# Kernel tuning notes

Measured on AMD Instinct MI355X. Metric: run time of the kernel, lower is better.

## Reference

```python
import math
import jax, jax.numpy as jnp
import numpy as np

N_HEAD = 16
ROPE_BASE = 10000.0


def _rope_tables(T, half, dtype):
    # build_sin_cos(seq_len, dim=head_dim//2): inv freq of length `half`
    pos = jnp.arange(T, dtype=jnp.float32)[:, None]                      # [T,1]
    inv = jnp.exp(jnp.arange(0, half * 2, 2, dtype=jnp.float32) * (-math.log(ROPE_BASE) / (half * 2)))  # [half]
    ang = pos * inv                                                       # [T,half]
    return jnp.sin(ang).astype(dtype), jnp.cos(ang).astype(dtype)


def setup_inputs() -> dict:
    key = jax.random.key(0)
    k1, k2, k3 = jax.random.split(key, 3)
    B, T, C = 2, 2048, 2048
    x = jax.random.normal(k1, (B, T, C), dtype=jnp.float32)
    w_qkv = jax.random.normal(k2, (3 * C, C), dtype=jnp.float32) * (1.0 / math.sqrt(C))
    w_proj = jax.random.normal(k3, (C, C), dtype=jnp.float32) * (1.0 / math.sqrt(C))
    return {"x": x, "w_qkv": w_qkv, "w_proj": w_proj}


def reference(x, w_qkv, w_proj):
    B, T, C = x.shape
    H = N_HEAD
    D = C // H
    half = D // 2

    qkv = jnp.einsum('btc,fc->btf', x, w_qkv).reshape(B, T, 3, H, D)
    q, k, v = qkv[:, :, 0], qkv[:, :, 1], qkv[:, :, 2]   # [B,T,H,D]

    sin, cos = _rope_tables(T, half, x.dtype)            # [T,half]
    sin = sin[None, :, None, :]                          # [1,T,1,half]
    cos = cos[None, :, None, :]

    def rot(t):
        t1, t2 = t[..., :half], t[..., half:]
        return jnp.concatenate([t1 * cos - t2 * sin, t2 * cos + t1 * sin], axis=-1)

    q, k = rot(q), rot(k)

    scale = 1.0 / math.sqrt(D)
    scores = jnp.einsum('bthd,bshd->bhts', q, k) * scale  # [B,H,T,T]
    causal = jnp.tril(jnp.ones((T, T), dtype=bool))
    scores = jnp.where(causal[None, None], scores, jnp.finfo(scores.dtype).min)
    probs = jax.nn.softmax(scores, axis=-1)
    out = jnp.einsum('bhts,bshd->bhtd', probs, v)         # [B,H,T,D]

    # Faithful to torch: view(B,T,H,D).permute(0,2,1,3).reshape_as(x)
    # flash output is token-major (B,T,H,D); permute gives (B,H,T,D), then flat reshape to (B,T,C).
    out = out.reshape(B, T, C)
    return jnp.einsum('btc,oc->bto', out, w_proj)
```

## Files before the change

kernel.cpp:

```cpp
#include <hip/hip_runtime.h>
#include <math.h>

typedef __attribute__((ext_vector_type(8))) short short8;
typedef __attribute__((ext_vector_type(4))) float f32x4;
typedef __attribute__((ext_vector_type(16))) float f32x16;
typedef __attribute__((ext_vector_type(4))) unsigned short ushort4v;
typedef __attribute__((ext_vector_type(2))) int int2v;

#define AS1 __attribute__((address_space(1)))
#define AS3 __attribute__((address_space(3)))
#define GLOAD16(src, dst) __builtin_amdgcn_global_load_lds((const AS1 void*)(src), (AS3 void*)(dst), 16, 0, 0)
#define VMWAIT(N) asm volatile("s_waitcnt vmcnt(" #N ")" ::: "memory")
#define LGKM0()   asm volatile("s_waitcnt lgkmcnt(0)" ::: "memory")

__device__ __forceinline__ unsigned short f2b(float f) {
    union { float f; unsigned int u; } c; c.f = f;
    return (unsigned short)((c.u + 0x7FFFu + ((c.u >> 16) & 1u)) >> 16);
}
__device__ __forceinline__ float b2f(unsigned short u) {
    union { unsigned int u; float f; } c; c.u = ((unsigned int)u) << 16;
    return c.f;
}
__device__ __forceinline__ int cvt_pk_bf16(float a, float b) {
    int r;
    asm("v_cvt_pk_bf16_f32 %0, %1, %2" : "=v"(r) : "v"(a), "v"(b));
    return r;
}
__device__ __forceinline__ int xcd_swz(int id, int nwg) {
    int q = nwg >> 3, r = nwg & 7, x = id & 7, rest = id >> 3;
    return (x < r ? x * (q + 1) : r * (q + 1) + (x - r) * q) + rest;
}

__global__ void cvt2(const float* __restrict__ a, const float* __restrict__ bsrc,
                     unsigned short* __restrict__ dst, int n4a) {
    int f = blockIdx.x * 256 + threadIdx.x;
    float4 v = (f < n4a) ? ((const float4*)a)[f] : ((const float4*)bsrc)[f - n4a];
    ushort4v o;
    o.x = f2b(v.x); o.y = f2b(v.y); o.z = f2b(v.z); o.w = f2b(v.w);
    ((ushort4v*)dst)[f] = o;
}

__global__ __launch_bounds__(256) void mid_fused(unsigned short* __restrict__ qkv,
                                                 unsigned short* __restrict__ vtg,
                                                 const float* __restrict__ wproj,
                                                 unsigned short* __restrict__ wpb) {
    int bid = blockIdx.x;
    if (bid < 16384) {
        int tid = bid * 256 + threadIdx.x;
        int i = tid & 63;
        int h = (tid >> 6) & 15;
        int t = (tid >> 10) & 2047;
        int b = tid >> 21;
        float inv = __expf((float)i * -0.14391156608f);
        float ang = (float)t * inv;
        float sn = sinf(ang), cs = cosf(ang);
        size_t base0 = ((size_t)(((b << 11) + t) * 3)) << 11;
#pragma unroll
        for (int s = 0; s < 2; ++s) {
            size_t base = base0 + (size_t)s * 2048 + (h << 7);
            float v1 = b2f(qkv[base + i]);
            float v2 = b2f(qkv[base + 64 + i]);
            qkv[base + i]      = f2b(v1 * cs - v2 * sn);
            qkv[base + 64 + i] = f2b(v2 * cs + v1 * sn);
        }
    } else if (bid < 16384 + 4096) {
        int flat = (bid - 16384) * 256 + threadIdx.x;
        int t = flat & 2047;
        int dc = (flat >> 11) & 15;
        int h = (flat >> 15) & 15;
        int b = flat >> 19;
        short8 v = *(const short8*)(qkv + ((size_t)(b * 2048 + t) * 3 + 2) * 2048 + h * 128 + dc * 8);
        size_t base = ((size_t)(b * 16 + h) * 128 + dc * 8) * 2048 + t;
#pragma unroll
        for (int j = 0; j < 8; j++) vtg[base + (size_t)j * 2048] = (unsigned short)v[j];
    } else {
        int f = (bid - 20480) * 256 + threadIdx.x;
#pragma unroll
        for (int r = 0; r < 4; ++r, f += 1024 * 256) {
            float4 v = ((const float4*)wproj)[f];
            ushort4v o;
            o.x = f2b(v.x); o.y = f2b(v.y); o.z = f2b(v.z); o.w = f2b(v.w);
            ((ushort4v*)wpb)[f] = o;
        }
    }
}

template<int OUT_BF16>
__global__ __launch_bounds__(512, 2) void gemm_nt(const unsigned short* __restrict__ A,
                                                  const unsigned short* __restrict__ B,
                                                  void* __restrict__ Cout,
                                                  int N, int K) {
    __shared__ __attribute__((aligned(16))) char lds[73728];
    int tid = threadIdx.x, lane = tid & 63, w = tid >> 6;
    int col = lane & 15, lg = lane >> 4;
    int wr = w >> 2, wc = w & 3;
    int gx = gridDim.x;
    int nwg = gx * gridDim.y;
    int id = xcd_swz(blockIdx.y * gx + blockIdx.x, nwg);
    int rowBase = (id / gx) * 128;
    int colBase = (id % gx) * 256;
    int nkt = K >> 5;

    f32x4 acc[4][4];
#pragma unroll
    for (int m = 0; m < 4; m++)
#pragma unroll
        for (int n = 0; n < 4; n++) acc[m][n] = (f32x4){0.f, 0.f, 0.f, 0.f};

    auto slotOf = [&](int t) { return t - (t / 3) * 3; };

    auto stageA = [&](int t) {
        char* dst = lds + slotOf(t) * 8192 + w * 1024;
        int u = w * 64 + lane;
        int row = u >> 2, ch = u & 3;
        const char* src = (const char*)A + ((size_t)(rowBase + row) * K + t * 32) * 2
                          + (((ch ^ (row >> 1)) & 3) << 4);
        GLOAD16(src, dst);
    };
    auto stageB = [&](int t) {
        char* base = lds + 24576 + slotOf(t) * 16384;
#pragma unroll
        for (int j = 0; j < 2; ++j) {
            int u = j * 512 + w * 64 + lane;
            int row = u >> 2, ch = u & 3;
            const char* src = (const char*)B + ((size_t)(colBase + row) * K + t * 32) * 2
                              + (((ch ^ (row >> 1)) & 3) << 4);
            GLOAD16(src, base + j * 8192 + w * 1024);
        }
    };

    stageA(0); stageB(0); stageA(1); stageB(1);

    for (int t = 0; t < nkt; ++t) {
        if (t + 1 < nkt) VMWAIT(3);
        else             VMWAIT(0);
        __builtin_amdgcn_s_barrier();
        if (t + 2 < nkt) { stageA(t + 2); stageB(t + 2); }
        const char* Ab = lds + slotOf(t) * 8192;
        const char* Bb = lds + 24576 + slotOf(t) * 16384;
        short8 af[4], bf[4];
#pragma unroll
        for (int m = 0; m < 4; ++m) {
            int row = wr * 64 + m * 16 + col;
            af[m] = *(const short8*)(Ab + row * 64 + (((lg ^ (row >> 1)) & 3) << 4));
        }
#pragma unroll
        for (int n = 0; n < 4; ++n) {
            int row = wc * 64 + n * 16 + col;
            bf[n] = *(const short8*)(Bb + row * 64 + (((lg ^ (row >> 1)) & 3) << 4));
        }
        __builtin_amdgcn_s_setprio(1);
#pragma unroll
        for (int m = 0; m < 4; ++m)
#pragma unroll
            for (int n = 0; n < 4; ++n)
                acc[m][n] = __builtin_amdgcn_mfma_f32_16x16x32_bf16(af[m], bf[n], acc[m][n], 0, 0, 0);
        __builtin_amdgcn_s_setprio(0);
        LGKM0();
    }

    int rbase = 4 * lg;
#pragma unroll
    for (int m = 0; m < 4; m++)
#pragma unroll
        for (int reg = 0; reg < 4; ++reg) {
            int r = rowBase + wr * 64 + m * 16 + rbase + reg;
#pragma unroll
            for (int n = 0; n < 4; n++) {
                int c = colBase + wc * 64 + n * 16 + col;
                float v = acc[m][n][reg];
                if (OUT_BF16) ((unsigned short*)Cout)[(size_t)r * N + c] = f2b(v);
                else          ((float*)Cout)[(size_t)r * N + c] = v;
            }
        }
}

__global__ __launch_bounds__(256, 2) void attn_fused(const unsigned short* __restrict__ qkv,
                                                     const unsigned short* __restrict__ vtg,
                                                     unsigned short* __restrict__ out) {
    constexpr int T = 2048;
    __shared__ unsigned short Kl[2][64 * 128];
    __shared__ unsigned short Vl[2][128 * 64];
    int tid = threadIdx.x, lane = tid & 63, w = tid >> 6;
    int q = lane & 31, hi = lane >> 5;
    int id = blockIdx.x;
    int bh = id & 31;
    int u = (id >> 5) & 7;
    int qt = (id >> 8) ? (15 - u) : u;
    int b = bh >> 4, h = bh & 15;
    const float sc2 = 0.08838834764831845f * 1.44269504088896340f;

    int qbase = qt * 128;
    int nkv = 2 * qt + 2;
    int tq = qbase + w * 32 + q;

    short8 qf[8];
    {
        const unsigned short* qp = qkv + ((size_t)(b * T + tq) * 3) * 2048 + h * 128;
#pragma unroll
        for (int s = 0; s < 8; s++) qf[s] = *(const short8*)(qp + s * 16 + hi * 8);
    }
    f32x16 O[4];
#pragma unroll
    for (int dt = 0; dt < 4; dt++)
#pragma unroll
        for (int r = 0; r < 16; r++) O[dt][r] = 0.f;
    float m = -1e30f, l = 0.f;

    auto stageK = [&](int t) {
        int kvb = t * 64;
        char* Kb = (char*)&Kl[t & 1][0];
#pragma unroll
        for (int it = 0; it < 4; ++it) {
            int dby = it * 4096 + tid * 16;
            int row = dby >> 8, cb = dby & 255;
            int scb = cb ^ ((row & 7) << 4);
            const char* src = (const char*)qkv + (((size_t)(b * T + kvb + row) * 3 + 1) * 2048 + h * 128) * 2 + scb;
            GLOAD16(src, Kb + it * 4096 + w * 1024);
        }
    };
    auto stageV = [&](int t) {
        int kvb = t * 64;
        char* Vb = (char*)&Vl[t & 1][0];
#pragma unroll
        for (int it = 0; it < 4; ++it) {
            int dby = it * 4096 + tid * 16;
            int d = dby >> 7, cb = dby & 127;
            int scb = cb ^ ((d & 7) << 4);
            const char* src = (const char*)vtg + (((size_t)bh * 128 + d) * 2048 + kvb) * 2 + scb;
            GLOAD16(src, Vb + it * 4096 + w * 1024);
        }
    };

    stageK(0); stageV(0);

    for (int kv = 0; kv < nkv; ++kv) {
        if (kv + 1 < nkv) {
            stageK(kv + 1);
            stageV(kv + 1);
            VMWAIT(8);
        } else {
            VMWAIT(0);
        }
        __builtin_amdgcn_s_barrier();
        int kvbase = kv * 64;
        bool act = kvbase < qbase + (w + 1) * 32;
        const char* Kb = (const char*)&Kl[kv & 1][0];
        const char* Vb = (const char*)&Vl[kv & 1][0];
        if (act) {
            f32x16 p0, p1;
#pragma unroll
            for (int r = 0; r < 16; r++) { p0[r] = 0.f; p1[r] = 0.f; }
            __builtin_amdgcn_s_setprio(1);
#pragma unroll
            for (int s = 0; s < 8; s++) {
                int cb = s * 32 + hi * 16;
                short8 k0 = *(const short8*)(Kb + q * 256 + (cb ^ ((q & 7) << 4)));
                p0 = __builtin_amdgcn_mfma_f32_32x32x16_bf16(k0, qf[s], p0, 0, 0, 0);
                short8 k1 = *(const short8*)(Kb + (32 + q) * 256 + (cb ^ ((q & 7) << 4)));
                p1 = __builtin_amdgcn_mfma_f32_32x32x16_bf16(k1, qf[s], p1, 0, 0, 0);
            }
            __builtin_amdgcn_s_setprio(0);
#pragma unroll
            for (int r = 0; r < 16; r++) { p0[r] *= sc2; p1[r] *= sc2; }
            bool diag = (kvbase + 63 > qbase + w * 32);
            if (diag) {
#pragma unroll
                for (int r = 0; r < 16; r++) {
                    int kg = kvbase + (r & 3) + 8 * (r >> 2) + 4 * hi;
                    if (kg > tq) p0[r] = -3e38f;
                    if (kg + 32 > tq) p1[r] = -3e38f;
                }
            }
            float mx = -3e38f;
#pragma unroll
            for (int r = 0; r < 16; r++) mx = fmaxf(mx, fmaxf(p0[r], p1[r]));
            mx = fmaxf(mx, __shfl_xor(mx, 32));
            if (!__all(mx - m <= 8.0f)) {
                float mn = fmaxf(m, mx);
                float esc = exp2f(m - mn);
                m = mn;
                l *= esc;
#pragma unroll
                for (int dt = 0; dt < 4; dt++)
#pragma unroll
                    for (int r = 0; r < 16; r++) O[dt][r] *= esc;
            }
            float rs = 0.f;
#pragma unroll
            for (int r = 0; r < 16; r++) {
                p0[r] = exp2f(p0[r] - m); rs += p0[r];
                p1[r] = exp2f(p1[r] - m); rs += p1[r];
            }
            rs += __shfl_xor(rs, 32);
            l += rs;
            union Frag { int i[4]; short8 s; } pa[4];
#pragma unroll
            for (int g = 0; g < 4; g++) {
                float e[8];
#pragma unroll
                for (int j = 0; j < 8; j++) e[j] = (g < 2) ? p0[(g & 1) * 8 + j] : p1[(g & 1) * 8 + j];
                int a0 = cvt_pk_bf16(e[0], e[1]);
                int a1 = cvt_pk_bf16(e[2], e[3]);
                int b0 = cvt_pk_bf16(e[4], e[5]);
                int b1 = cvt_pk_bf16(e[6], e[7]);
                int s0 = hi ? a0 : b0; int r0 = __shfl_xor(s0, 32);
                int s1 = hi ? a1 : b1; int r1 = __shfl_xor(s1, 32);
                pa[g].i[0] = hi ? r0 : a0;
                pa[g].i[1] = hi ? r1 : a1;
                pa[g].i[2] = hi ? b0 : r0;
                pa[g].i[3] = hi ? b1 : r1;
            }
            __builtin_amdgcn_s_setprio(1);
#pragma unroll
            for (int dt = 0; dt < 4; dt++) {
                int d = dt * 32 + q;
#pragma unroll
                for (int ks = 0; ks < 4; ks++) {
                    short8 vfr = *(const short8*)(Vb + d * 128 + ((ks * 32 + hi * 16) ^ ((d & 7) << 4)));
                    O[dt] = __builtin_amdgcn_mfma_f32_32x32x16_bf16(vfr, pa[ks].s, O[dt], 0, 0, 0);
                }
            }
            __builtin_amdgcn_s_setprio(0);
        }
        LGKM0();
        __builtin_amdgcn_s_barrier();
    }
    float linv = 1.0f / l;
    size_t obase = ((size_t)bh * T + tq) * 128;
#pragma unroll
    for (int dt = 0; dt < 4; dt++)
#pragma unroll
        for (int g = 0; g < 4; g++) {
            int d0 = dt * 32 + g * 8 + 4 * hi;
            int w0 = cvt_pk_bf16(O[dt][4 * g + 0] * linv, O[dt][4 * g + 1] * linv);
            int w1 = cvt_pk_bf16(O[dt][4 * g + 2] * linv, O[dt][4 * g + 3] * linv);
            int2v o; o[0] = w0; o[1] = w1;
            *(int2v*)(out + obase + d0) = o;
        }
}

extern "C" void kernel_launch(void* const* d_in, const int* in_sizes, int n_in,
                              void* d_out, int out_size, void* d_ws, size_t ws_size,
                              hipStream_t stream) {
    const float* x      = (const float*)d_in[0];
    const float* w_qkv  = (const float*)d_in[1];
    const float* w_proj = (const float*)d_in[2];
    const int B = 2, T = 2048, C = 2048;
    const int M = B * T;
    const int F = 3 * C;

    size_t need = ((size_t)M * C + (size_t)F * C + (size_t)M * F) * 2;
    if (ws_size < need) return;
    unsigned short* rX  = (unsigned short*)d_ws;
    unsigned short* rW  = rX + (size_t)M * C;
    unsigned short* rQ  = rW + (size_t)F * C;
    unsigned short* rVT = rW;
    unsigned short* rWp = rW + (size_t)B * 16 * 128 * T;

    cvt2<<<(M * C + F * C) / 1024, 256, 0, stream>>>(x, w_qkv, rX, (M * C) / 4);
    gemm_nt<1><<<dim3(F / 256, M / 128), 512, 0, stream>>>(rX, rW, (void*)rQ, F, C);
    mid_fused<<<16384 + 4096 + 1024, 256, 0, stream>>>(rQ, rVT, w_proj, rWp);
    attn_fused<<<512, 256, 0, stream>>>(rQ, rVT, rX);
    gemm_nt<0><<<dim3(C / 256, M / 128), 512, 0, stream>>>(rX, rWp, d_out, C, C);
}
```

Measured before the change: 271.9 us.

## Vectorize RoPE and V-transpose passes, hoist K/V staging, split softmax reductions

The RoPE section now has each thread process four elements with 8-byte loads and stores, which cuts the block count by four. The V-transpose section handles two tokens per thread and writes 4-byte pairs instead of scattered 2-byte stores. In the attention kernel, the first K/V async loads are issued before the Q fragment load and accumulator init, so those latencies overlap. The row-max and row-sum reductions are restructured into trees and multiple accumulators to shorten dependency chains. Sin/cos is still recomputed per element, so the transcendental work in RoPE is unchanged.

```diff
diff --git a/kernel.cpp b/kernel.cpp
--- a/kernel.cpp
+++ b/kernel.cpp
@@ -5,6 +5,7 @@
 typedef __attribute__((ext_vector_type(4))) float f32x4;
 typedef __attribute__((ext_vector_type(16))) float f32x16;
 typedef __attribute__((ext_vector_type(4))) unsigned short ushort4v;
+typedef __attribute__((ext_vector_type(2))) unsigned short ushort2v;
 typedef __attribute__((ext_vector_type(2))) int int2v;
 
 #define AS1 __attribute__((address_space(1)))
@@ -45,36 +46,50 @@
                                                  const float* __restrict__ wproj,
                                                  unsigned short* __restrict__ wpb) {
     int bid = blockIdx.x;
-    if (bid < 16384) {
+    if (bid < 4096) {
         int tid = bid * 256 + threadIdx.x;
-        int i = tid & 63;
-        int h = (tid >> 6) & 15;
-        int t = (tid >> 10) & 2047;
-        int b = tid >> 21;
-        float inv = __expf((float)i * -0.14391156608f);
-        float ang = (float)t * inv;
-        float sn = sinf(ang), cs = cosf(ang);
+        int i4 = (tid & 15) << 2;
+        int h = (tid >> 4) & 15;
+        int t = (tid >> 8) & 2047;
+        int b = tid >> 19;
         size_t base0 = ((size_t)(((b << 11) + t) * 3)) << 11;
 #pragma unroll
         for (int s = 0; s < 2; ++s) {
             size_t base = base0 + (size_t)s * 2048 + (h << 7);
-            float v1 = b2f(qkv[base + i]);
-            float v2 = b2f(qkv[base + 64 + i]);
-            qkv[base + i]      = f2b(v1 * cs - v2 * sn);
-            qkv[base + 64 + i] = f2b(v2 * cs + v1 * sn);
-        }
-    } else if (bid < 16384 + 4096) {
-        int flat = (bid - 16384) * 256 + threadIdx.x;
-        int t = flat & 2047;
-        int dc = (flat >> 11) & 15;
-        int h = (flat >> 15) & 15;
-        int b = flat >> 19;
-        short8 v = *(const short8*)(qkv + ((size_t)(b * 2048 + t) * 3 + 2) * 2048 + h * 128 + dc * 8);
+            ushort4v v1 = *(const ushort4v*)(qkv + base + i4);
+            ushort4v v2 = *(const ushort4v*)(qkv + base + 64 + i4);
+            ushort4v o1, o2;
+#pragma unroll
+            for (int j = 0; j < 4; ++j) {
+                int i = i4 + j;
+                float inv = __expf((float)i * -0.14391156608f);
+                float ang = (float)t * inv;
+                float sn = sinf(ang), cs = cosf(ang);
+                float a1 = b2f(v1[j]), a2 = b2f(v2[j]);
+                o1[j] = f2b(a1 * cs - a2 * sn);
+                o2[j] = f2b(a2 * cs + a1 * sn);
+            }
+            *(ushort4v*)(qkv + base + i4) = o1;
+            *(ushort4v*)(qkv + base + 64 + i4) = o2;
+        }
+    } else if (bid < 4096 + 2048) {
+        int flat = (bid - 4096) * 256 + threadIdx.x;
+        int t2 = flat & 1023;
+        int dc = (flat >> 10) & 15;
+        int h = (flat >> 14) & 15;
+        int b = flat >> 18;
+        int t = t2 << 1;
+        const unsigned short* src = qkv + ((size_t)(b * 2048 + t) * 3 + 2) * 2048 + h * 128 + dc * 8;
+        short8 v0 = *(const short8*)src;
+        short8 v1 = *(const short8*)(src + 3 * 2048);
         size_t base = ((size_t)(b * 16 + h) * 128 + dc * 8) * 2048 + t;
 #pragma unroll
-        for (int j = 0; j < 8; j++) vtg[base + (size_t)j * 2048] = (unsigned short)v[j];
+        for (int j = 0; j < 8; j++) {
+            ushort2v o; o[0] = (unsigned short)v0[j]; o[1] = (unsigned short)v1[j];
+            *(ushort2v*)(vtg + base + (size_t)j * 2048) = o;
+        }
     } else {
-        int f = (bid - 20480) * 256 + threadIdx.x;
+        int f = (bid - 6144) * 256 + threadIdx.x;
 #pragma unroll
         for (int r = 0; r < 4; ++r, f += 1024 * 256) {
             float4 v = ((const float4*)wproj)[f];
@@ -194,19 +209,6 @@
     int nkv = 2 * qt + 2;
     int tq = qbase + w * 32 + q;
 
-    short8 qf[8];
-    {
-        const unsigned short* qp = qkv + ((size_t)(b * T + tq) * 3) * 2048 + h * 128;
-#pragma unroll
-        for (int s = 0; s < 8; s++) qf[s] = *(const short8*)(qp + s * 16 + hi * 8);
-    }
-    f32x16 O[4];
-#pragma unroll
-    for (int dt = 0; dt < 4; dt++)
-#pragma unroll
-        for (int r = 0; r < 16; r++) O[dt][r] = 0.f;
-    float m = -1e30f, l = 0.f;
-
     auto stageK = [&](int t) {
         int kvb = t * 64;
         char* Kb = (char*)&Kl[t & 1][0];
@@ -233,6 +235,19 @@
     };
 
     stageK(0); stageV(0);
+
+    short8 qf[8];
+    {
+        const unsigned short* qp = qkv + ((size_t)(b * T + tq) * 3) * 2048 + h * 128;
+#pragma unroll
+        for (int s = 0; s < 8; s++) qf[s] = *(const short8*)(qp + s * 16 + hi * 8);
+    }
+    f32x16 O[4];
+#pragma unroll
+    for (int dt = 0; dt < 4; dt++)
+#pragma unroll
+        for (int r = 0; r < 16; r++) O[dt][r] = 0.f;
+    float m = -1e30f, l = 0.f;
 
     for (int kv = 0; kv < nkv; ++kv) {
         if (kv + 1 < nkv) {
@@ -272,9 +287,14 @@
                     if (kg + 32 > tq) p1[r] = -3e38f;
                 }
             }
-            float mx = -3e38f;
-#pragma unroll
-            for (int r = 0; r < 16; r++) mx = fmaxf(mx, fmaxf(p0[r], p1[r]));
+            float tr[16];
+#pragma unroll
+            for (int r = 0; r < 16; r++) tr[r] = fmaxf(p0[r], p1[r]);
+#pragma unroll
+            for (int r = 0; r < 8; r++) tr[r] = fmaxf(tr[r], tr[r + 8]);
+#pragma unroll
+            for (int r = 0; r < 4; r++) tr[r] = fmaxf(tr[r], tr[r + 4]);
+            float mx = fmaxf(fmaxf(tr[0], tr[1]), fmaxf(tr[2], tr[3]));
             mx = fmaxf(mx, __shfl_xor(mx, 32));
             if (!__all(mx - m <= 8.0f)) {
                 float mn = fmaxf(m, mx);
@@ -286,12 +306,19 @@
 #pragma unroll
                     for (int r = 0; r < 16; r++) O[dt][r] *= esc;
             }
-            float rs = 0.f;
-#pragma unroll
-            for (int r = 0; r < 16; r++) {
-                p0[r] = exp2f(p0[r] - m); rs += p0[r];
-                p1[r] = exp2f(p1[r] - m); rs += p1[r];
-            }
+            float s0 = 0.f, s1 = 0.f, s2 = 0.f, s3 = 0.f;
+#pragma unroll
+            for (int r = 0; r < 16; r += 4) {
+                p0[r]     = exp2f(p0[r]     - m); s0 += p0[r];
+                p0[r + 1] = exp2f(p0[r + 1] - m); s1 += p0[r + 1];
+                p0[r + 2] = exp2f(p0[r + 2] - m); s2 += p0[r + 2];
+                p0[r + 3] = exp2f(p0[r + 3] - m); s3 += p0[r + 3];
+                p1[r]     = exp2f(p1[r]     - m); s0 += p1[r];
+                p1[r + 1] = exp2f(p1[r + 1] - m); s1 += p1[r + 1];
+                p1[r + 2] = exp2f(p1[r + 2] - m); s2 += p1[r + 2];
+                p1[r + 3] = exp2f(p1[r + 3] - m); s3 += p1[r + 3];
+            }
+            float rs = (s0 + s1) + (s2 + s3);
             rs += __shfl_xor(rs, 32);
             l += rs;
             union Frag { int i[4]; short8 s; } pa[4];
@@ -304,8 +331,8 @@
                 int a1 = cvt_pk_bf16(e[2], e[3]);
                 int b0 = cvt_pk_bf16(e[4], e[5]);
                 int b1 = cvt_pk_bf16(e[6], e[7]);
-                int s0 = hi ? a0 : b0; int r0 = __shfl_xor(s0, 32);
-                int s1 = hi ? a1 : b1; int r1 = __shfl_xor(s1, 32);
+                int s0i = hi ? a0 : b0; int r0 = __shfl_xor(s0i, 32);
+                int s1i = hi ? a1 : b1; int r1 = __shfl_xor(s1i, 32);
                 pa[g].i[0] = hi ? r0 : a0;
                 pa[g].i[1] = hi ? r1 : a1;
                 pa[g].i[2] = hi ? b0 : r0;
@@ -360,7 +387,7 @@
 
     cvt2<<<(M * C + F * C) / 1024, 256, 0, stream>>>(x, w_qkv, rX, (M * C) / 4);
     gemm_nt<1><<<dim3(F / 256, M / 128), 512, 0, stream>>>(rX, rW, (void*)rQ, F, C);
-    mid_fused<<<16384 + 4096 + 1024, 256, 0, stream>>>(rQ, rVT, w_proj, rWp);
+    mid_fused<<<4096 + 2048 + 1024, 256, 0, stream>>>(rQ, rVT, w_proj, rWp);
     attn_fused<<<512, 256, 0, stream>>>(rQ, rVT, rX);
     gemm_nt<0><<<dim3(C / 256, M / 128), 512, 0, stream>>>(rX, rWp, d_out, C, C);
 }
```

Result: no change. 273.4 us (+0.6%).
